# Kernel tuning notes

Hardware: AMD Instinct MI355X
Metric: run time of the kernel (lower is better)

## Reference

```python
import jax, jax.numpy as jnp
import numpy as np

LEAKY_SLOPE = 0.2

def gcn_conv(x, W, b, src, dst, deg_inv_sqrt, num_nodes):
    # GCNConv: out = D^{-1/2} (A+I) D^{-1/2} X W + b
    h = x @ W                                   # [N, out]
    norm = deg_inv_sqrt[src] * deg_inv_sqrt[dst]  # [E']
    msg = h[src] * norm[:, None]                # gather + scale
    out = jax.ops.segment_sum(msg, dst, num_segments=num_nodes)
    return out + b

def gcn_forward(x, edge_index, W1, b1, W2, b2, W3, b3):
    num_nodes = x.shape[0]
    loop = jnp.arange(num_nodes, dtype=edge_index.dtype)
    src = jnp.concatenate([edge_index[0], loop])  # add self-loops
    dst = jnp.concatenate([edge_index[1], loop])
    deg = jax.ops.segment_sum(jnp.ones_like(dst, dtype=x.dtype), dst,
                              num_segments=num_nodes)
    deg_inv_sqrt = jnp.where(deg > 0, jax.lax.rsqrt(deg), 0.0)
    # dropout is identity in eval mode (training=False)
    h = gcn_conv(x, W1, b1, src, dst, deg_inv_sqrt, num_nodes)
    h = jax.nn.leaky_relu(h, negative_slope=LEAKY_SLOPE)
    h = gcn_conv(h, W2, b2, src, dst, deg_inv_sqrt, num_nodes)
    h = jax.nn.leaky_relu(h, negative_slope=LEAKY_SLOPE)
    h = gcn_conv(h, W3, b3, src, dst, deg_inv_sqrt, num_nodes)
    return h

def setup_inputs() -> dict:
    key = jax.random.key(0)
    ks = jax.random.split(key, 8)
    N, F, E, C = 100000, 256, 3200000, 40
    x = jax.random.normal(ks[0], (N, F), dtype=jnp.float32)
    edge_index = jax.random.randint(ks[1], (2, E), 0, N, dtype=jnp.int64)
    W1 = jax.random.normal(ks[2], (F, 128), dtype=jnp.float32) * (1.0 / np.sqrt(F))
    b1 = jnp.zeros((128,), dtype=jnp.float32)
    W2 = jax.random.normal(ks[3], (128, 16), dtype=jnp.float32) * (1.0 / np.sqrt(128))
    b2 = jnp.zeros((16,), dtype=jnp.float32)
    W3 = jax.random.normal(ks[4], (16, C), dtype=jnp.float32) * (1.0 / np.sqrt(16))
    b3 = jnp.zeros((C,), dtype=jnp.float32)
    return {"x": x, "edge_index": edge_index, "W1": W1, "b1": b1,
            "W2": W2, "b2": b2, "W3": W3, "b3": b3}

def reference(x, edge_index, W1, b1, W2, b2, W3, b3):
    return gcn_forward(x, edge_index, W1, b1, W2, b2, W3, b3)
```

## Files before the change

kernel.cpp:

```cpp
#include <hip/hip_runtime.h>
#include <hip/hip_fp16.h>
#include <math.h>

#define LEAKY 0.2f
#define BP 6
#define BSZ 64
#define NBUK_MAX 2048

typedef _Float16 f16x8 __attribute__((ext_vector_type(8)));
typedef float f32x4 __attribute__((ext_vector_type(4)));

union H2 { __half2 h; int i; };
union H8 { __half2 h[4]; float4 f; };
union H4 { __half2 h[2]; float2 f; };

__device__ inline __half2 shfl_xor_h2(__half2 v, int m) {
    H2 u; u.h = v;
    u.i = __shfl_xor(u.i, m);
    return u.h;
}

__global__ __launch_bounds__(256) void kinit(const int* __restrict__ dst,
                                             int* __restrict__ bhist,
                                             int* __restrict__ bhB,
                                             int E, int nbuk, int chunk,
                                             const float* __restrict__ W1,
                                             __half* __restrict__ W1t) {
    if (blockIdx.x < 256) {
        __shared__ int hist[NBUK_MAX];
        int t = threadIdx.x;
        for (int i = t; i < nbuk; i += 256) hist[i] = 0;
        __syncthreads();
        int base = blockIdx.x * chunk;
        int end = min(base + chunk, E);
        for (int e = base + t; e < end; e += 256)
            atomicAdd(&hist[dst[e] >> BP], 1);
        __syncthreads();
        int* myrow = bhB + (size_t)blockIdx.x * nbuk;
        for (int i = t; i < nbuk; i += 256) {
            int v = hist[i];
            myrow[i] = v;
            if (v) atomicAdd(&bhist[i], v);
        }
    } else {
        int idx = (blockIdx.x - 256) * 256 + threadIdx.x;
        if (idx < 32768) {
            int n = idx >> 8, k = idx & 255;
            W1t[idx] = __float2half(W1[k * 128 + n]);
        }
    }
}

__global__ __launch_bounds__(1024) void bscan(const int* __restrict__ bhist,
                                              int* __restrict__ bbase,
                                              int* __restrict__ bcur, int nbuk) {
    __shared__ int s[1024];
    int t = threadIdx.x;
    int v[4]; int sum = 0;
    #pragma unroll
    for (int i = 0; i < 4; ++i) {
        int idx = t * 4 + i;
        v[i] = (idx < nbuk) ? bhist[idx] : 0;
        sum += v[i];
    }
    s[t] = sum; __syncthreads();
    for (int off = 1; off < 1024; off <<= 1) {
        int a = (t >= off) ? s[t - off] : 0;
        __syncthreads();
        s[t] += a;
        __syncthreads();
    }
    int run = (t > 0) ? s[t - 1] : 0;
    #pragma unroll
    for (int i = 0; i < 4; ++i) {
        int idx = t * 4 + i;
        if (idx < nbuk) { bbase[idx] = run; bcur[idx] = run; run += v[i]; }
    }
    if (t == 1023) bbase[nbuk] = s[1023];
}

__global__ __launch_bounds__(256) void kscatter2(const int* __restrict__ src,
                                                 const int* __restrict__ dst,
                                                 int* __restrict__ bcur,
                                                 const int* __restrict__ bhB,
                                                 int* __restrict__ ebuf,
                                                 int E, int nbuk, int chunk) {
    __shared__ int hist[NBUK_MAX];
    int t = threadIdx.x;
    int base = blockIdx.x * chunk;
    int end = min(base + chunk, E);
    const int* myrow = bhB + (size_t)blockIdx.x * nbuk;
    for (int i = t; i < nbuk; i += 256) {
        int c = myrow[i];
        hist[i] = c ? atomicAdd(&bcur[i], c) : 0;
    }
    __syncthreads();
    for (int e = base + t; e < end; e += 256) {
        int d = dst[e];
        int pos = atomicAdd(&hist[d >> BP], 1);
        ebuf[pos] = ((d & (BSZ - 1)) << 17) | src[e];
    }
}

__global__ __launch_bounds__(256) void kbuild(const int* __restrict__ ebuf,
                                              const int* __restrict__ bbase,
                                              int* __restrict__ rowptr,
                                              float* __restrict__ dis,
                                              int* __restrict__ col, int N) {
    __shared__ int h[BSZ];
    __shared__ int cur[BSZ];
    int b = blockIdx.x, t = threadIdx.x;
    if (t < BSZ) h[t] = 0;
    __syncthreads();
    int beg = bbase[b], end = bbase[b + 1];
    for (int j = beg + t; j < end; j += 256)
        atomicAdd(&h[(ebuf[j] >> 17) & (BSZ - 1)], 1);
    __syncthreads();
    if (t < BSZ) {
        int node = b * BSZ + t;
        int c = (node < N) ? h[t] + 1 : 0;
        int incl = c;
        #pragma unroll
        for (int off = 1; off < 64; off <<= 1) {
            int v = __shfl_up(incl, off);
            if (t >= off) incl += v;
        }
        int colbase = beg + b * BSZ;
        if (node < N) {
            int r = colbase + incl - c;
            rowptr[node] = r;
            dis[node] = rsqrtf((float)c);
            col[r] = node;
            cur[t] = r + 1;
            if (node == N - 1) rowptr[N] = colbase + incl;
        }
    }
    __syncthreads();
    for (int j = beg + t; j < end; j += 256) {
        int v = ebuf[j];
        int p = atomicAdd(&cur[(v >> 17) & (BSZ - 1)], 1);
        col[p] = v & 0x1FFFF;
    }
}

__global__ __launch_bounds__(256) void gemm1_mfma(
        const float* __restrict__ x, const __half* __restrict__ W1t,
        const float* __restrict__ dis, __half* __restrict__ C, int M) {
    int wave = threadIdx.x >> 6;
    int lane = threadIdx.x & 63;
    int m = lane & 15, q = lane >> 4;
    int row0 = (blockIdx.x * 4 + wave) * 16;
    int arow = row0 + m;
    bool aval = arow < M;
    const float* xr = x + (size_t)arow * 256 + q * 8;
    f32x4 acc[8];
    #pragma unroll
    for (int c = 0; c < 8; ++c) acc[c] = (f32x4){0.f, 0.f, 0.f, 0.f};
    for (int k0 = 0; k0 < 256; k0 += 32) {
        f16x8 a;
        if (aval) {
            float4 v0 = *(const float4*)(xr + k0);
            float4 v1 = *(const float4*)(xr + k0 + 4);
            a[0] = (_Float16)v0.x; a[1] = (_Float16)v0.y;
            a[2] = (_Float16)v0.z; a[3] = (_Float16)v0.w;
            a[4] = (_Float16)v1.x; a[5] = (_Float16)v1.y;
            a[6] = (_Float16)v1.z; a[7] = (_Float16)v1.w;
        } else {
            #pragma unroll
            for (int i = 0; i < 8; ++i) a[i] = (_Float16)0.f;
        }
        #pragma unroll
        for (int c = 0; c < 8; ++c) {
            f16x8 b = *(const f16x8*)(W1t + (size_t)(c * 16 + m) * 256 + k0 + q * 8);
            acc[c] = __builtin_amdgcn_mfma_f32_16x16x32_f16(a, b, acc[c], 0, 0, 0);
        }
    }
    float dw[4];
    #pragma unroll
    for (int r = 0; r < 4; ++r) {
        int rr = row0 + q * 4 + r;
        dw[r] = (rr < M) ? dis[rr] : 0.f;
    }
    #pragma unroll
    for (int c = 0; c < 8; ++c) {
        #pragma unroll
        for (int r = 0; r < 4; ++r) {
            int rr = row0 + q * 4 + r;
            if (rr < M)
                C[(size_t)rr * 128 + c * 16 + m] = __float2half(acc[c][r] * dw[r]);
        }
    }
}

__global__ __launch_bounds__(256) void prop128g2(
        const __half* __restrict__ h, const int* __restrict__ rowptr,
        const int* __restrict__ col, const float* __restrict__ dis,
        const float* __restrict__ bias, const float* __restrict__ W2,
        __half* __restrict__ out, int N) {
    __shared__ float sw[2048];
    for (int k = threadIdx.x; k < 2048; k += 256) {
        int f  = k >> 8;
        int r  = k & 255;
        int e2 = r >> 6;
        int qq = (r >> 2) & 15;
        int jj = r & 3;
        sw[k] = W2[(qq * 8 + f) * 16 + e2 * 4 + jj];
    }
    __syncthreads();

    int n = (blockIdx.x * 256 + threadIdx.x) >> 6;
    if (n >= N) return;
    int lane = threadIdx.x & 63;
    int eo = lane >> 4;
    int q = lane & 15;
    const float4* __restrict__ h4 = (const float4*)h;
    int beg = rowptr[n], end = rowptr[n + 1];
    __half2 acc[4];
    acc[0] = acc[1] = acc[2] = acc[3] = __float2half2_rn(0.f);
    int j = beg + eo;
    for (; j + 28 < end; j += 32) {
        int s0 = col[j],      s1 = col[j + 4],  s2 = col[j + 8],  s3 = col[j + 12];
        int s4 = col[j + 16], s5 = col[j + 20], s6 = col[j + 24], s7 = col[j + 28];
        H8 u0, u1, u2, u3, u4, u5, u6, u7;
        u0.f = h4[(size_t)s0 * 16 + q];
        u1.f = h4[(size_t)s1 * 16 + q];
        u2.f = h4[(size_t)s2 * 16 + q];
        u3.f = h4[(size_t)s3 * 16 + q];
        u4.f = h4[(size_t)s4 * 16 + q];
        u5.f = h4[(size_t)s5 * 16 + q];
        u6.f = h4[(size_t)s6 * 16 + q];
        u7.f = h4[(size_t)s7 * 16 + q];
        #pragma unroll
        for (int i = 0; i < 4; ++i) acc[i] = __hadd2(acc[i], u0.h[i]);
        #pragma unroll
        for (int i = 0; i < 4; ++i) acc[i] = __hadd2(acc[i], u1.h[i]);
        #pragma unroll
        for (int i = 0; i < 4; ++i) acc[i] = __hadd2(acc[i], u2.h[i]);
        #pragma unroll
        for (int i = 0; i < 4; ++i) acc[i] = __hadd2(acc[i], u3.h[i]);
        #pragma unroll
        for (int i = 0; i < 4; ++i) acc[i] = __hadd2(acc[i], u4.h[i]);
        #pragma unroll
        for (int i = 0; i < 4; ++i) acc[i] = __hadd2(acc[i], u5.h[i]);
        #pragma unroll
        for (int i = 0; i < 4; ++i) acc[i] = __hadd2(acc[i], u6.h[i]);
        #pragma unroll
        for (int i = 0; i < 4; ++i) acc[i] = __hadd2(acc[i], u7.h[i]);
    }
    for (; j + 12 < end; j += 16) {
        int s0 = col[j], s1 = col[j + 4], s2 = col[j + 8], s3 = col[j + 12];
        H8 u0, u1, u2, u3;
        u0.f = h4[(size_t)s0 * 16 + q];
        u1.f = h4[(size_t)s1 * 16 + q];
        u2.f = h4[(size_t)s2 * 16 + q];
        u3.f = h4[(size_t)s3 * 16 + q];
        #pragma unroll
        for (int i = 0; i < 4; ++i) acc[i] = __hadd2(acc[i], u0.h[i]);
        #pragma unroll
        for (int i = 0; i < 4; ++i) acc[i] = __hadd2(acc[i], u1.h[i]);
        #pragma unroll
        for (int i = 0; i < 4; ++i) acc[i] = __hadd2(acc[i], u2.h[i]);
        #pragma unroll
        for (int i = 0; i < 4; ++i) acc[i] = __hadd2(acc[i], u3.h[i]);
    }
    for (; j + 4 < end; j += 8) {
        int s0 = col[j], s1 = col[j + 4];
        H8 u0, u1;
        u0.f = h4[(size_t)s0 * 16 + q];
        u1.f = h4[(size_t)s1 * 16 + q];
        #pragma unroll
        for (int i = 0; i < 4; ++i) acc[i] = __hadd2(acc[i], u0.h[i]);
        #pragma unroll
        for (int i = 0; i < 4; ++i) acc[i] = __hadd2(acc[i], u1.h[i]);
    }
    for (; j < end; j += 4) {
        int s = col[j];
        H8 u; u.f = h4[(size_t)s * 16 + q];
        #pragma unroll
        for (int i = 0; i < 4; ++i) acc[i] = __hadd2(acc[i], u.h[i]);
    }
    #pragma unroll
    for (int i = 0; i < 4; ++i) {
        acc[i] = __hadd2(acc[i], shfl_xor_h2(acc[i], 16));
        acc[i] = __hadd2(acc[i], shfl_xor_h2(acc[i], 32));
    }
    float dn = dis[n];
    const float4* b4 = (const float4*)bias;
    float4 bA = b4[q * 2];
    float4 bB = b4[q * 2 + 1];
    float2 f0 = __half22float2(acc[0]);
    float2 f1 = __half22float2(acc[1]);
    float2 f2 = __half22float2(acc[2]);
    float2 f3 = __half22float2(acc[3]);
    float xf[8];
    xf[0] = fmaf(dn, f0.x, bA.x); xf[1] = fmaf(dn, f0.y, bA.y);
    xf[2] = fmaf(dn, f1.x, bA.z); xf[3] = fmaf(dn, f1.y, bA.w);
    xf[4] = fmaf(dn, f2.x, bB.x); xf[5] = fmaf(dn, f2.y, bB.y);
    xf[6] = fmaf(dn, f3.x, bB.z); xf[7] = fmaf(dn, f3.y, bB.w);
    #pragma unroll
    for (int i = 0; i < 8; ++i) xf[i] = xf[i] > 0.f ? xf[i] : LEAKY * xf[i];
    float p0 = 0.f, p1 = 0.f, p2 = 0.f, p3 = 0.f;
    #pragma unroll
    for (int f = 0; f < 8; ++f) {
        f32x4 wv = *(const f32x4*)&sw[f * 256 + eo * 64 + q * 4];
        p0 = fmaf(xf[f], wv[0], p0);
        p1 = fmaf(xf[f], wv[1], p1);
        p2 = fmaf(xf[f], wv[2], p2);
        p3 = fmaf(xf[f], wv[3], p3);
    }
    #pragma unroll
    for (int mm = 1; mm < 16; mm <<= 1) {
        p0 += __shfl_xor(p0, mm);
        p1 += __shfl_xor(p1, mm);
        p2 += __shfl_xor(p2, mm);
        p3 += __shfl_xor(p3, mm);
    }
    if (q == 0) {
        H4 w;
        w.h[0] = __floats2half2_rn(p0 * dn, p1 * dn);
        w.h[1] = __floats2half2_rn(p2 * dn, p3 * dn);
        ((float2*)out)[(size_t)n * 4 + eo] = w.f;
    }
}

__global__ __launch_bounds__(256) void prop16(
        const __half* __restrict__ h, const int* __restrict__ rowptr,
        const int* __restrict__ col, const float* __restrict__ dis,
        const float* __restrict__ bias, __half* __restrict__ outp, int N) {
    int t = blockIdx.x * 256 + threadIdx.x;
    int n = t >> 4;
    if (n >= N) return;
    int li = threadIdx.x & 15;
    int eo = li >> 3;
    int hq = li & 7;
    const int* __restrict__ h2i = (const int*)h;
    int beg = rowptr[n], end = rowptr[n + 1];
    __half2 acc = __float2half2_rn(0.f);
    int j = beg + eo;
    for (; j + 14 < end; j += 16) {
        H2 u0, u1, u2, u3, u4, u5, u6, u7;
        u0.i = h2i[(size_t)col[j]      * 8 + hq];
        u1.i = h2i[(size_t)col[j + 2]  * 8 + hq];
        u2.i = h2i[(size_t)col[j + 4]  * 8 + hq];
        u3.i = h2i[(size_t)col[j + 6]  * 8 + hq];
        u4.i = h2i[(size_t)col[j + 8]  * 8 + hq];
        u5.i = h2i[(size_t)col[j + 10] * 8 + hq];
        u6.i = h2i[(size_t)col[j + 12] * 8 + hq];
        u7.i = h2i[(size_t)col[j + 14] * 8 + hq];
        acc = __hadd2(acc, u0.h); acc = __hadd2(acc, u1.h);
        acc = __hadd2(acc, u2.h); acc = __hadd2(acc, u3.h);
        acc = __hadd2(acc, u4.h); acc = __hadd2(acc, u5.h);
        acc = __hadd2(acc, u6.h); acc = __hadd2(acc, u7.h);
    }
    for (; j + 6 < end; j += 8) {
        H2 u0, u1, u2, u3;
        u0.i = h2i[(size_t)col[j]     * 8 + hq];
        u1.i = h2i[(size_t)col[j + 2] * 8 + hq];
        u2.i = h2i[(size_t)col[j + 4] * 8 + hq];
        u3.i = h2i[(size_t)col[j + 6] * 8 + hq];
        acc = __hadd2(acc, u0.h); acc = __hadd2(acc, u1.h);
        acc = __hadd2(acc, u2.h); acc = __hadd2(acc, u3.h);
    }
    for (; j < end; j += 2) {
        H2 u; u.i = h2i[(size_t)col[j] * 8 + hq];
        acc = __hadd2(acc, u.h);
    }
    acc = __hadd2(acc, shfl_xor_h2(acc, 8));
    if (eo == 0) {
        float dn = dis[n];
        float2 f = __half22float2(acc);
        float ox = fmaf(dn, f.x, bias[hq * 2]);
        float oy = fmaf(dn, f.y, bias[hq * 2 + 1]);
        ox = ox > 0.f ? ox : LEAKY * ox;
        oy = oy > 0.f ? oy : LEAKY * oy;
        ox *= dn; oy *= dn;
        H2 w; w.h = __floats2half2_rn(ox, oy);
        ((int*)outp)[(size_t)n * 8 + hq] = w.i;
    }
}

__global__ __launch_bounds__(256) void prop16_gemm3(
        const __half* __restrict__ h, const int* __restrict__ rowptr,
        const int* __restrict__ col, const float* __restrict__ dis,
        const float* __restrict__ W3, const float* __restrict__ b3,
        float* __restrict__ out, int N) {
    __shared__ float sw[640];
    __shared__ float sb[40];
    int t0 = threadIdx.x;
    for (int i = t0; i < 640; i += 256) sw[i] = W3[i];
    if (t0 < 40) sb[t0] = b3[t0];
    __syncthreads();
    int t = blockIdx.x * 256 + t0;
    int n = t >> 4;
    if (n >= N) return;
    int li = t0 & 15;
    int eo = li >> 3;
    int hq = li & 7;
    const int* __restrict__ h2i = (const int*)h;
    int beg = rowptr[n], end = rowptr[n + 1];
    __half2 acc = __float2half2_rn(0.f);
    int j = beg + eo;
    for (; j + 14 < end; j += 16) {
        H2 u0, u1, u2, u3, u4, u5, u6, u7;
        u0.i = h2i[(size_t)col[j]      * 8 + hq];
        u1.i = h2i[(size_t)col[j + 2]  * 8 + hq];
        u2.i = h2i[(size_t)col[j + 4]  * 8 + hq];
        u3.i = h2i[(size_t)col[j + 6]  * 8 + hq];
        u4.i = h2i[(size_t)col[j + 8]  * 8 + hq];
        u5.i = h2i[(size_t)col[j + 10] * 8 + hq];
        u6.i = h2i[(size_t)col[j + 12] * 8 + hq];
        u7.i = h2i[(size_t)col[j + 14] * 8 + hq];
        acc = __hadd2(acc, u0.h); acc = __hadd2(acc, u1.h);
        acc = __hadd2(acc, u2.h); acc = __hadd2(acc, u3.h);
        acc = __hadd2(acc, u4.h); acc = __hadd2(acc, u5.h);
        acc = __hadd2(acc, u6.h); acc = __hadd2(acc, u7.h);
    }
    for (; j + 6 < end; j += 8) {
        H2 u0, u1, u2, u3;
        u0.i = h2i[(size_t)col[j]     * 8 + hq];
        u1.i = h2i[(size_t)col[j + 2] * 8 + hq];
        u2.i = h2i[(size_t)col[j + 4] * 8 + hq];
        u3.i = h2i[(size_t)col[j + 6] * 8 + hq];
        acc = __hadd2(acc, u0.h); acc = __hadd2(acc, u1.h);
        acc = __hadd2(acc, u2.h); acc = __hadd2(acc, u3.h);
    }
    for (; j < end; j += 2) {
        H2 u; u.i = h2i[(size_t)col[j] * 8 + hq];
        acc = __hadd2(acc, u.h);
    }
    acc = __hadd2(acc, shfl_xor_h2(acc, 8));
    float dn = dis[n];
    int slot = (t0 & 63) & ~15;
    H2 av; av.h = acc;
    float oA = 0.f, oB = 0.f, oC = 0.f;
    #pragma unroll
    for (int hh = 0; hh < 8; ++hh) {
        H2 u; u.i = __shfl(av.i, slot + hh);
        float2 p = __half22float2(u.h);
        float p0 = dn * p.x, p1 = dn * p.y;
        int k0 = hh * 2;
        oA = fmaf(p0, sw[k0 * 40 + li],            oA);
        oA = fmaf(p1, sw[(k0 + 1) * 40 + li],      oA);
        oB = fmaf(p0, sw[k0 * 40 + li + 16],       oB);
        oB = fmaf(p1, sw[(k0 + 1) * 40 + li + 16], oB);
        if (li < 8) {
            oC = fmaf(p0, sw[k0 * 40 + li + 32],       oC);
            oC = fmaf(p1, sw[(k0 + 1) * 40 + li + 32], oC);
        }
    }
    float* orow = out + (size_t)n * 40;
    orow[li]      = oA + sb[li];
    orow[li + 16] = oB + sb[li + 16];
    if (li < 8) orow[li + 32] = oC + sb[li + 32];
}


extern "C" void kernel_launch(void* const* d_in, const int* in_sizes, int n_in,
                              void* d_out, int out_size, void* d_ws, size_t ws_size,
                              hipStream_t stream) {
    const float* x  = (const float*)d_in[0];
    const int*   ei = (const int*)d_in[1];
    const float* W1 = (const float*)d_in[2];
    const float* b1 = (const float*)d_in[3];
    const float* W2 = (const float*)d_in[4];
    const float* b2 = (const float*)d_in[5];
    const float* W3 = (const float*)d_in[6];
    const float* b3 = (const float*)d_in[7];
    float* out = (float*)d_out;

    int N = in_sizes[0] / 256;
    int E = in_sizes[1] / 2;
    const int* src = ei;
    const int* dst = ei + E;
    int NBUK = (N + BSZ - 1) >> BP;

    char* w = (char*)d_ws;
    auto alloc = [&](size_t bytes) {
        char* p = w;
        w += (bytes + 255) & ~(size_t)255;
        return p;
    };
    int*    rowptr  = (int*)   alloc((size_t)(N + 1) * 4);
    int*    bhist   = (int*)   alloc((size_t)NBUK * 4);
    int*    bbase   = (int*)   alloc((size_t)(NBUK + 1) * 4);
    int*    bcur    = (int*)   alloc((size_t)NBUK * 4);
    int*    bhB     = (int*)   alloc((size_t)256 * NBUK * 4);
    int*    ebuf    = (int*)   alloc((size_t)E * 4);
    int*    colx    = (int*)   alloc((size_t)(E + N) * 4);
    float*  dis     = (float*) alloc((size_t)N * 4);
    __half* W1t     = (__half*)alloc((size_t)128 * 256 * 2);
    __half* h1h     = (__half*)alloc((size_t)N * 128 * 2);
    __half* h2h     = (__half*)alloc((size_t)N * 16 * 2);
    __half* x2h     = (__half*)alloc((size_t)N * 16 * 2);

    int SC_BLOCKS = 256;
    int chunk = (E + SC_BLOCKS - 1) / SC_BLOCKS;

    (void)hipMemsetAsync(bhist, 0, (size_t)NBUK * 4, stream);
    kinit   <<<384, 256, 0, stream>>>(dst, bhist, bhB, E, NBUK, chunk, W1, W1t);
    bscan   <<<1, 1024, 0, stream>>>(bhist, bbase, bcur, NBUK);
    kscatter2<<<SC_BLOCKS, 256, 0, stream>>>(src, dst, bcur, bhB, ebuf, E, NBUK, chunk);
    kbuild  <<<NBUK, 256, 0, stream>>>(ebuf, bbase, rowptr, dis, colx, N);

    int gtiles = (N + 63) / 64;
    gemm1_mfma<<<gtiles, 256, 0, stream>>>(x, W1t, dis, h1h, N);
    prop128g2 <<<(N * 64 + 255) / 256, 256, 0, stream>>>(h1h, rowptr, colx,
                                                         dis, b1, W2, h2h, N);
    prop16    <<<(N * 16 + 255) / 256, 256, 0, stream>>>(h2h, rowptr, colx,
                                                         dis, b2, x2h, N);
    prop16_gemm3<<<(N * 16 + 255) / 256, 256, 0, stream>>>(x2h, rowptr, colx,
                                                           dis, W3, b3, out, N);
}
```

Baseline: 523.6 us.

## Use 16-byte gathers with 8 threads per node in 16-wide propagation kernels

The two 16-feature propagation kernels now assign 8 threads per node instead of 16, and each thread loads half a row (8 halfs) as one float4 rather than a 4-byte half2. Four edge slots per node are reduced with xor shuffles. The fused gemm3 epilogue is reworked so each of the 8 lanes computes 5 output columns from all 16 features exchanged via a shuffle. This halves the thread count and issues fewer, wider gather instructions for the irregular neighbor reads, but gives less edge-level parallelism per node and more registers per thread.

```diff
diff --git a/kernel.cpp b/kernel.cpp
--- a/kernel.cpp
+++ b/kernel.cpp
@@ -328,54 +328,78 @@
         const int* __restrict__ col, const float* __restrict__ dis,
         const float* __restrict__ bias, __half* __restrict__ outp, int N) {
     int t = blockIdx.x * 256 + threadIdx.x;
-    int n = t >> 4;
+    int n = t >> 3;
     if (n >= N) return;
-    int li = threadIdx.x & 15;
-    int eo = li >> 3;
-    int hq = li & 7;
-    const int* __restrict__ h2i = (const int*)h;
+    int li = threadIdx.x & 7;
+    int slot = li >> 1;
+    int half = li & 1;
+    const float4* __restrict__ h4 = (const float4*)h;
     int beg = rowptr[n], end = rowptr[n + 1];
-    __half2 acc = __float2half2_rn(0.f);
-    int j = beg + eo;
-    for (; j + 14 < end; j += 16) {
-        H2 u0, u1, u2, u3, u4, u5, u6, u7;
-        u0.i = h2i[(size_t)col[j]      * 8 + hq];
-        u1.i = h2i[(size_t)col[j + 2]  * 8 + hq];
-        u2.i = h2i[(size_t)col[j + 4]  * 8 + hq];
-        u3.i = h2i[(size_t)col[j + 6]  * 8 + hq];
-        u4.i = h2i[(size_t)col[j + 8]  * 8 + hq];
-        u5.i = h2i[(size_t)col[j + 10] * 8 + hq];
-        u6.i = h2i[(size_t)col[j + 12] * 8 + hq];
-        u7.i = h2i[(size_t)col[j + 14] * 8 + hq];
-        acc = __hadd2(acc, u0.h); acc = __hadd2(acc, u1.h);
-        acc = __hadd2(acc, u2.h); acc = __hadd2(acc, u3.h);
-        acc = __hadd2(acc, u4.h); acc = __hadd2(acc, u5.h);
-        acc = __hadd2(acc, u6.h); acc = __hadd2(acc, u7.h);
-    }
-    for (; j + 6 < end; j += 8) {
-        H2 u0, u1, u2, u3;
-        u0.i = h2i[(size_t)col[j]     * 8 + hq];
-        u1.i = h2i[(size_t)col[j + 2] * 8 + hq];
-        u2.i = h2i[(size_t)col[j + 4] * 8 + hq];
-        u3.i = h2i[(size_t)col[j + 6] * 8 + hq];
-        acc = __hadd2(acc, u0.h); acc = __hadd2(acc, u1.h);
-        acc = __hadd2(acc, u2.h); acc = __hadd2(acc, u3.h);
-    }
-    for (; j < end; j += 2) {
-        H2 u; u.i = h2i[(size_t)col[j] * 8 + hq];
-        acc = __hadd2(acc, u.h);
-    }
-    acc = __hadd2(acc, shfl_xor_h2(acc, 8));
-    if (eo == 0) {
+    __half2 acc[4];
+    acc[0] = acc[1] = acc[2] = acc[3] = __float2half2_rn(0.f);
+    int j = beg + slot;
+    for (; j + 12 < end; j += 16) {
+        int s0 = col[j], s1 = col[j + 4], s2 = col[j + 8], s3 = col[j + 12];
+        H8 u0, u1, u2, u3;
+        u0.f = h4[(size_t)s0 * 2 + half];
+        u1.f = h4[(size_t)s1 * 2 + half];
+        u2.f = h4[(size_t)s2 * 2 + half];
+        u3.f = h4[(size_t)s3 * 2 + half];
+        #pragma unroll
+        for (int i = 0; i < 4; ++i) acc[i] = __hadd2(acc[i], u0.h[i]);
+        #pragma unroll
+        for (int i = 0; i < 4; ++i) acc[i] = __hadd2(acc[i], u1.h[i]);
+        #pragma unroll
+        for (int i = 0; i < 4; ++i) acc[i] = __hadd2(acc[i], u2.h[i]);
+        #pragma unroll
+        for (int i = 0; i < 4; ++i) acc[i] = __hadd2(acc[i], u3.h[i]);
+    }
+    for (; j + 4 < end; j += 8) {
+        int s0 = col[j], s1 = col[j + 4];
+        H8 u0, u1;
+        u0.f = h4[(size_t)s0 * 2 + half];
+        u1.f = h4[(size_t)s1 * 2 + half];
+        #pragma unroll
+        for (int i = 0; i < 4; ++i) acc[i] = __hadd2(acc[i], u0.h[i]);
+        #pragma unroll
+        for (int i = 0; i < 4; ++i) acc[i] = __hadd2(acc[i], u1.h[i]);
+    }
+    for (; j < end; j += 4) {
+        int s = col[j];
+        H8 u; u.f = h4[(size_t)s * 2 + half];
+        #pragma unroll
+        for (int i = 0; i < 4; ++i) acc[i] = __hadd2(acc[i], u.h[i]);
+    }
+    #pragma unroll
+    for (int i = 0; i < 4; ++i) {
+        acc[i] = __hadd2(acc[i], shfl_xor_h2(acc[i], 2));
+        acc[i] = __hadd2(acc[i], shfl_xor_h2(acc[i], 4));
+    }
+    if (slot == 0) {
         float dn = dis[n];
-        float2 f = __half22float2(acc);
-        float ox = fmaf(dn, f.x, bias[hq * 2]);
-        float oy = fmaf(dn, f.y, bias[hq * 2 + 1]);
-        ox = ox > 0.f ? ox : LEAKY * ox;
-        oy = oy > 0.f ? oy : LEAKY * oy;
-        ox *= dn; oy *= dn;
-        H2 w; w.h = __floats2half2_rn(ox, oy);
-        ((int*)outp)[(size_t)n * 8 + hq] = w.i;
+        const float4* b4 = (const float4*)bias;
+        float4 bA = b4[half * 2];
+        float4 bB = b4[half * 2 + 1];
+        float2 f0 = __half22float2(acc[0]);
+        float2 f1 = __half22float2(acc[1]);
+        float2 f2 = __half22float2(acc[2]);
+        float2 f3 = __half22float2(acc[3]);
+        float o0 = fmaf(dn, f0.x, bA.x), o1 = fmaf(dn, f0.y, bA.y);
+        float o2 = fmaf(dn, f1.x, bA.z), o3 = fmaf(dn, f1.y, bA.w);
+        float o4 = fmaf(dn, f2.x, bB.x), o5 = fmaf(dn, f2.y, bB.y);
+        float o6 = fmaf(dn, f3.x, bB.z), o7 = fmaf(dn, f3.y, bB.w);
+        o0 = o0 > 0.f ? o0 : LEAKY * o0;  o1 = o1 > 0.f ? o1 : LEAKY * o1;
+        o2 = o2 > 0.f ? o2 : LEAKY * o2;  o3 = o3 > 0.f ? o3 : LEAKY * o3;
+        o4 = o4 > 0.f ? o4 : LEAKY * o4;  o5 = o5 > 0.f ? o5 : LEAKY * o5;
+        o6 = o6 > 0.f ? o6 : LEAKY * o6;  o7 = o7 > 0.f ? o7 : LEAKY * o7;
+        o0 *= dn; o1 *= dn; o2 *= dn; o3 *= dn;
+        o4 *= dn; o5 *= dn; o6 *= dn; o7 *= dn;
+        H8 w;
+        w.h[0] = __floats2half2_rn(o0, o1);
+        w.h[1] = __floats2half2_rn(o2, o3);
+        w.h[2] = __floats2half2_rn(o4, o5);
+        w.h[3] = __floats2half2_rn(o6, o7);
+        ((float4*)outp)[(size_t)n * 2 + half] = w.f;
     }
 }
 
@@ -391,67 +415,83 @@
     if (t0 < 40) sb[t0] = b3[t0];
     __syncthreads();
     int t = blockIdx.x * 256 + t0;
-    int n = t >> 4;
+    int n = t >> 3;
     if (n >= N) return;
-    int li = t0 & 15;
-    int eo = li >> 3;
-    int hq = li & 7;
-    const int* __restrict__ h2i = (const int*)h;
+    int li = t0 & 7;
+    int slot = li >> 1;
+    int half = li & 1;
+    const float4* __restrict__ h4 = (const float4*)h;
     int beg = rowptr[n], end = rowptr[n + 1];
-    __half2 acc = __float2half2_rn(0.f);
-    int j = beg + eo;
-    for (; j + 14 < end; j += 16) {
-        H2 u0, u1, u2, u3, u4, u5, u6, u7;
-        u0.i = h2i[(size_t)col[j]      * 8 + hq];
-        u1.i = h2i[(size_t)col[j + 2]  * 8 + hq];
-        u2.i = h2i[(size_t)col[j + 4]  * 8 + hq];
-        u3.i = h2i[(size_t)col[j + 6]  * 8 + hq];
-        u4.i = h2i[(size_t)col[j + 8]  * 8 + hq];
-        u5.i = h2i[(size_t)col[j + 10] * 8 + hq];
-        u6.i = h2i[(size_t)col[j + 12] * 8 + hq];
-        u7.i = h2i[(size_t)col[j + 14] * 8 + hq];
-        acc = __hadd2(acc, u0.h); acc = __hadd2(acc, u1.h);
-        acc = __hadd2(acc, u2.h); acc = __hadd2(acc, u3.h);
-        acc = __hadd2(acc, u4.h); acc = __hadd2(acc, u5.h);
-        acc = __hadd2(acc, u6.h); acc = __hadd2(acc, u7.h);
-    }
-    for (; j + 6 < end; j += 8) {
-        H2 u0, u1, u2, u3;
-        u0.i = h2i[(size_t)col[j]     * 8 + hq];
-        u1.i = h2i[(size_t)col[j + 2] * 8 + hq];
-        u2.i = h2i[(size_t)col[j + 4] * 8 + hq];
-        u3.i = h2i[(size_t)col[j + 6] * 8 + hq];
-        acc = __hadd2(acc, u0.h); acc = __hadd2(acc, u1.h);
-        acc = __hadd2(acc, u2.h); acc = __hadd2(acc, u3.h);
-    }
-    for (; j < end; j += 2) {
-        H2 u; u.i = h2i[(size_t)col[j] * 8 + hq];
-        acc = __hadd2(acc, u.h);
-    }
-    acc = __hadd2(acc, shfl_xor_h2(acc, 8));
+    __half2 acc[4];
+    acc[0] = acc[1] = acc[2] = acc[3] = __float2half2_rn(0.f);
+    int j = beg + slot;
+    for (; j + 12 < end; j += 16) {
+        int s0 = col[j], s1 = col[j + 4], s2 = col[j + 8], s3 = col[j + 12];
+        H8 u0, u1, u2, u3;
+        u0.f = h4[(size_t)s0 * 2 + half];
+        u1.f = h4[(size_t)s1 * 2 + half];
+        u2.f = h4[(size_t)s2 * 2 + half];
+        u3.f = h4[(size_t)s3 * 2 + half];
+        #pragma unroll
+        for (int i = 0; i < 4; ++i) acc[i] = __hadd2(acc[i], u0.h[i]);
+        #pragma unroll
+        for (int i = 0; i < 4; ++i) acc[i] = __hadd2(acc[i], u1.h[i]);
+        #pragma unroll
+        for (int i = 0; i < 4; ++i) acc[i] = __hadd2(acc[i], u2.h[i]);
+        #pragma unroll
+        for (int i = 0; i < 4; ++i) acc[i] = __hadd2(acc[i], u3.h[i]);
+    }
+    for (; j + 4 < end; j += 8) {
+        int s0 = col[j], s1 = col[j + 4];
+        H8 u0, u1;
+        u0.f = h4[(size_t)s0 * 2 + half];
+        u1.f = h4[(size_t)s1 * 2 + half];
+        #pragma unroll
+        for (int i = 0; i < 4; ++i) acc[i] = __hadd2(acc[i], u0.h[i]);
+        #pragma unroll
+        for (int i = 0; i < 4; ++i) acc[i] = __hadd2(acc[i], u1.h[i]);
+    }
+    for (; j < end; j += 4) {
+        int s = col[j];
+        H8 u; u.f = h4[(size_t)s * 2 + half];
+        #pragma unroll
+        for (int i = 0; i < 4; ++i) acc[i] = __hadd2(acc[i], u.h[i]);
+    }
+    #pragma unroll
+    for (int i = 0; i < 4; ++i) {
+        acc[i] = __hadd2(acc[i], shfl_xor_h2(acc[i], 2));
+        acc[i] = __hadd2(acc[i], shfl_xor_h2(acc[i], 4));
+    }
+    __half2 oth[4];
+    #pragma unroll
+    for (int i = 0; i < 4; ++i) oth[i] = shfl_xor_h2(acc[i], 1);
     float dn = dis[n];
-    int slot = (t0 & 63) & ~15;
-    H2 av; av.h = acc;
-    float oA = 0.f, oB = 0.f, oC = 0.f;
-    #pragma unroll
-    for (int hh = 0; hh < 8; ++hh) {
-        H2 u; u.i = __shfl(av.i, slot + hh);
-        float2 p = __half22float2(u.h);
-        float p0 = dn * p.x, p1 = dn * p.y;
-        int k0 = hh * 2;
-        oA = fmaf(p0, sw[k0 * 40 + li],            oA);
-        oA = fmaf(p1, sw[(k0 + 1) * 40 + li],      oA);
-        oB = fmaf(p0, sw[k0 * 40 + li + 16],       oB);
-        oB = fmaf(p1, sw[(k0 + 1) * 40 + li + 16], oB);
-        if (li < 8) {
-            oC = fmaf(p0, sw[k0 * 40 + li + 32],       oC);
-            oC = fmaf(p1, sw[(k0 + 1) * 40 + li + 32], oC);
-        }
+    float p[16];
+    #pragma unroll
+    for (int i = 0; i < 4; ++i) {
+        __half2 lo = half ? oth[i] : acc[i];
+        __half2 hi = half ? acc[i] : oth[i];
+        float2 a = __half22float2(lo);
+        float2 b = __half22float2(hi);
+        p[2 * i]     = dn * a.x;  p[2 * i + 1]     = dn * a.y;
+        p[8 + 2 * i] = dn * b.x;  p[8 + 2 * i + 1] = dn * b.y;
+    }
+    float o0 = 0.f, o1 = 0.f, o2 = 0.f, o3 = 0.f, o4 = 0.f;
+    #pragma unroll
+    for (int k = 0; k < 16; ++k) {
+        const float* wr = &sw[k * 40 + li];
+        o0 = fmaf(p[k], wr[0],  o0);
+        o1 = fmaf(p[k], wr[8],  o1);
+        o2 = fmaf(p[k], wr[16], o2);
+        o3 = fmaf(p[k], wr[24], o3);
+        o4 = fmaf(p[k], wr[32], o4);
     }
     float* orow = out + (size_t)n * 40;
-    orow[li]      = oA + sb[li];
-    orow[li + 16] = oB + sb[li + 16];
-    if (li < 8) orow[li + 32] = oC + sb[li + 32];
+    orow[li]      = o0 + sb[li];
+    orow[li + 8]  = o1 + sb[li + 8];
+    orow[li + 16] = o2 + sb[li + 16];
+    orow[li + 24] = o3 + sb[li + 24];
+    orow[li + 32] = o4 + sb[li + 32];
 }
 
 
@@ -506,8 +546,8 @@
     gemm1_mfma<<<gtiles, 256, 0, stream>>>(x, W1t, dis, h1h, N);
     prop128g2 <<<(N * 64 + 255) / 256, 256, 0, stream>>>(h1h, rowptr, colx,
                                                          dis, b1, W2, h2h, N);
-    prop16    <<<(N * 16 + 255) / 256, 256, 0, stream>>>(h2h, rowptr, colx,
-                                                         dis, b2, x2h, N);
-    prop16_gemm3<<<(N * 16 + 255) / 256, 256, 0, stream>>>(x2h, rowptr, colx,
-                                                           dis, W3, b3, out, N);
-}
+    prop16    <<<(N * 8 + 255) / 256, 256, 0, stream>>>(h2h, rowptr, colx,
+                                                        dis, b2, x2h, N);
+    prop16_gemm3<<<(N * 8 + 255) / 256, 256, 0, stream>>>(x2h, rowptr, colx,
+                                                          dis, W3, b3, out, N);
+}
```

Result: no change. 517.2 us (-1.2%).
